# Performance work log

Measured on AMD Instinct MI355X. Metric: run time of the kernel, lower is better.

The kernel has to match this reference:

```python
import jax, jax.numpy as jnp
import numpy as np

B, S, HID = 2, 2048, 2048
H = 16
NOPE, ROPE, VD = 128, 64, 128
QHD = NOPE + ROPE  # 192
KV_RANK = 512
MAX_POS = 2048
EPS = 1e-6


def _rotate_half(x):
    d = x.shape[-1] // 2
    return jnp.concatenate([-x[..., d:], x[..., :d]], axis=-1)


def setup_inputs() -> dict:
    key = jax.random.key(0)
    ks = jax.random.split(key, 8)
    hidden_states = jax.random.normal(ks[0], (B, S, HID), dtype=jnp.float32)
    position_ids = jax.random.randint(ks[1], (B, S), 0, MAX_POS)
    # real RoPE tables
    inv_freq = 1.0 / (10000.0 ** (np.arange(0, ROPE, 2, dtype=np.float32) / ROPE))
    t = np.arange(MAX_POS, dtype=np.float32)
    freqs = np.outer(t, inv_freq)                      # [MAX_POS, ROPE/2]
    emb = np.concatenate([freqs, freqs], axis=-1)      # [MAX_POS, ROPE]
    cos = jnp.asarray(np.cos(emb), dtype=jnp.float32)
    sin = jnp.asarray(np.sin(emb), dtype=jnp.float32)
    sc = lambda fan_in: 1.0 / np.sqrt(fan_in)
    W_q = jax.random.normal(ks[2], (HID, H * QHD), dtype=jnp.float32) * sc(HID)
    W_kva = jax.random.normal(ks[3], (HID, KV_RANK + ROPE), dtype=jnp.float32) * sc(HID)
    ln_g = jnp.ones((KV_RANK,), dtype=jnp.float32)
    ln_b = jnp.zeros((KV_RANK,), dtype=jnp.float32)
    W_kvb = jax.random.normal(ks[4], (KV_RANK, H * (NOPE + VD)), dtype=jnp.float32) * sc(KV_RANK)
    W_o = jax.random.normal(ks[5], (H * VD, HID), dtype=jnp.float32) * sc(H * VD)
    return {"hidden_states": hidden_states, "position_ids": position_ids,
            "cos": cos, "sin": sin, "W_q": W_q, "W_kva": W_kva,
            "ln_g": ln_g, "ln_b": ln_b, "W_kvb": W_kvb, "W_o": W_o}


def _layernorm(x, g, b):
    mu = jnp.mean(x, axis=-1, keepdims=True)
    var = jnp.mean(jnp.square(x - mu), axis=-1, keepdims=True)
    return (x - mu) * jax.lax.rsqrt(var + EPS) * g + b


def reference(hidden_states, position_ids, cos, sin, W_q, W_kva, ln_g, ln_b, W_kvb, W_o):
    bsz, q_len, _ = hidden_states.shape
    # Q projection -> split nope/rope
    q = (hidden_states @ W_q).reshape(bsz, q_len, H, QHD)      # [b,s,h,192]
    q_nope, q_pe = q[..., :NOPE], q[..., NOPE:]
    # compressed KV + shared rope key
    ckv = hidden_states @ W_kva                                 # [b,s,512+64]
    compressed_kv, k_pe = ckv[..., :KV_RANK], ckv[..., KV_RANK:]
    k_pe = k_pe[:, :, None, :]                                  # [b,s,1,64]
    kv = (_layernorm(compressed_kv, ln_g, ln_b) @ W_kvb).reshape(bsz, q_len, H, NOPE + VD)
    k_nope, value_states = kv[..., :NOPE], kv[..., NOPE:]
    # RoPE
    cos_p = cos[position_ids][:, :, None, :]                    # [b,s,1,64]
    sin_p = sin[position_ids][:, :, None, :]
    q_pe = q_pe * cos_p + _rotate_half(q_pe) * sin_p
    k_pe = k_pe * cos_p + _rotate_half(k_pe) * sin_p
    query = jnp.concatenate([q_nope, q_pe], axis=-1)            # [b,s,h,192]
    key = jnp.concatenate([k_nope, jnp.broadcast_to(k_pe, k_nope.shape[:-1] + (ROPE,))], axis=-1)
    # causal attention (FlashMLA math, dense reference)
    scale = 1.0 / jnp.sqrt(jnp.float32(QHD))
    scores = jnp.einsum('bqhd,bkhd->bhqk', query, key) * scale  # [b,h,s,s]
    causal = jnp.tril(jnp.ones((q_len, q_len), dtype=bool))
    scores = jnp.where(causal[None, None], scores, jnp.finfo(scores.dtype).min)
    attn = jax.nn.softmax(scores, axis=-1)
    out = jnp.einsum('bhqk,bkhd->bqhd', attn, value_states)     # [b,s,h,128]
    out = out.reshape(bsz, q_len, H * VD)
    # NOTE: source applies o_proj twice (kept for faithfulness; HID == H*VD)
    out = out @ W_o
    out = out @ W_o
    return out
```

## Files before the change

### kernel.cpp

```cpp
#include <hip/hip_runtime.h>

typedef __bf16 bf16;
typedef __bf16 bf16x4 __attribute__((ext_vector_type(4)));
typedef __bf16 bf16x8 __attribute__((ext_vector_type(8)));
typedef float  f32x4  __attribute__((ext_vector_type(4)));

__device__ __forceinline__ f32x4 mfma16(bf16x8 a, bf16x8 b, f32x4 c) {
  return __builtin_amdgcn_mfma_f32_16x16x32_bf16(a, b, c, 0, 0, 0);
}
__device__ __forceinline__ void load_lds16(const void* g, void* l) {
  __builtin_amdgcn_global_load_lds((__attribute__((address_space(1))) void*)(g),
                                   (__attribute__((address_space(3))) void*)(l),
                                   16, 0, 0);
}

__global__ void cast_bf16(const float* __restrict__ s, bf16* __restrict__ d, int n4) {
  int i = blockIdx.x * blockDim.x + threadIdx.x;
  if (i < n4) {
    float4 v = ((const float4*)s)[i];
    bf16x4 o = { (bf16)v.x, (bf16)v.y, (bf16)v.z, (bf16)v.w };
    *(bf16x4*)(d + (size_t)i * 4) = o;
  }
}

__global__ void transpose_cast(const float* __restrict__ src, bf16* __restrict__ dst,
                               int K, int N, int Npad) {
  __shared__ float tile[32][33];
  const int n0 = blockIdx.x * 32, k0 = blockIdx.y * 32;
  const int tx = threadIdx.x, ty = threadIdx.y;
#pragma unroll
  for (int i = 0; i < 4; ++i) {
    int k = k0 + ty + i * 8, n = n0 + tx;
    tile[ty + i * 8][tx] = (k < K && n < N) ? src[(size_t)k * N + n] : 0.f;
  }
  __syncthreads();
#pragma unroll
  for (int i = 0; i < 4; ++i) {
    int n = n0 + ty + i * 8, k = k0 + tx;
    if (n < Npad && k < K) dst[(size_t)n * K + k] = (bf16)tile[tx][ty + i * 8];
  }
}

template <typename OutT>
__global__ __launch_bounds__(512) void gemm2_bt(
    const bf16* __restrict__ A, const bf16* __restrict__ Bt, OutT* __restrict__ C,
    int M, int N, int K, int GBM, int GBN) {
  __shared__ alignas(16) bf16 As[2][256 * 32];
  __shared__ alignas(16) bf16 Bs[2][128 * 32];
  const int wg = blockIdx.x;
  const int gsz = 8 * GBN;
  const int g = wg / gsz, rem = wg % gsz;
  const int bm = g * 8 + (rem % 8);
  const int bn = rem / 8;

  const int tid = threadIdx.x, wid = tid >> 6, lane = tid & 63;
  const int wr = wid >> 1, wc = wid & 1;
  const int lo = lane & 15, hi = lane >> 4;
  const int w64 = wid * 64;

  f32x4 acc[4][4];
#pragma unroll
  for (int m = 0; m < 4; ++m)
#pragma unroll
    for (int n = 0; n < 4; ++n) acc[m][n] = f32x4{0.f, 0.f, 0.f, 0.f};

  const bf16* Abase = A + (size_t)(bm * 256) * K;
  const bf16* Bbase = Bt + (size_t)(bn * 128) * K;

  auto stage = [&](int buf, int kt) {
    int c = w64 + lane;
    load_lds16(Abase + (size_t)(c >> 2) * K + kt + (c & 3) * 8,
               &As[buf][0] + (size_t)w64 * 8);
    int c2 = 512 + w64 + lane;
    load_lds16(Abase + (size_t)(c2 >> 2) * K + kt + (c2 & 3) * 8,
               &As[buf][0] + (size_t)(512 + w64) * 8);
    load_lds16(Bbase + (size_t)(c >> 2) * K + kt + (c & 3) * 8,
               &Bs[buf][0] + (size_t)w64 * 8);
  };

  const int nt = K >> 5;
  stage(0, 0);
  __syncthreads();
  int cur = 0;
  for (int t = 0; t < nt; ++t) {
    if (t + 1 < nt) stage(cur ^ 1, (t + 1) << 5);
    bf16x8 af[4], bfr[4];
#pragma unroll
    for (int m = 0; m < 4; ++m)
      af[m] = *(const bf16x8*)(&As[cur][0] + (size_t)(wr * 64 + m * 16 + lo) * 32 + hi * 8);
#pragma unroll
    for (int n = 0; n < 4; ++n)
      bfr[n] = *(const bf16x8*)(&Bs[cur][0] + (size_t)(wc * 64 + n * 16 + lo) * 32 + hi * 8);
#pragma unroll
    for (int m = 0; m < 4; ++m)
#pragma unroll
      for (int n = 0; n < 4; ++n) acc[m][n] = mfma16(af[m], bfr[n], acc[m][n]);
    __syncthreads();
    cur ^= 1;
  }
#pragma unroll
  for (int m = 0; m < 4; ++m)
#pragma unroll
    for (int n = 0; n < 4; ++n)
#pragma unroll
      for (int r = 0; r < 4; ++r) {
        int row = bm * 256 + wr * 64 + m * 16 + hi * 4 + r;
        int col = bn * 128 + wc * 64 + n * 16 + lo;
        C[(size_t)row * N + col] = (OutT)acc[m][n][r];
      }
}

template <typename OutT>
__global__ __launch_bounds__(256) void gemm1g_bt(
    const bf16* __restrict__ A, const bf16* __restrict__ Bt, OutT* __restrict__ C,
    int M, int N, int K, int GBN) {
  __shared__ alignas(16) bf16 As[128 * 32];
  __shared__ alignas(16) bf16 Bs[128 * 32];
  const int wg = blockIdx.x;
  const int gsz = 8 * GBN;
  const int g = wg / gsz, rem = wg % gsz;
  const int bm = g * 8 + (rem & 7);
  const int bn = rem >> 3;
  const int tid = threadIdx.x, wid = tid >> 6, lane = tid & 63;
  const int wr = wid >> 1, wc = wid & 1;
  const int lo = lane & 15, hi = lane >> 4;
  f32x4 acc[4][4];
#pragma unroll
  for (int m = 0; m < 4; ++m)
#pragma unroll
    for (int n = 0; n < 4; ++n) acc[m][n] = f32x4{0.f, 0.f, 0.f, 0.f};

  const bf16* Abase = A + (size_t)(bm * 128) * K;
  const bf16* Bbase = Bt + (size_t)(bn * 128) * K;

  for (int kt = 0; kt < K; kt += 32) {
    __syncthreads();
    for (int c0 = wid * 64; c0 < 512; c0 += 256) {
      int c = c0 + lane;
      int row = c >> 2, kc = c & 3;
      load_lds16(Abase + (size_t)row * K + kt + kc * 8, As + (size_t)c0 * 8);
      load_lds16(Bbase + (size_t)row * K + kt + kc * 8, Bs + (size_t)c0 * 8);
    }
    __syncthreads();
    bf16x8 af[4], bfr[4];
#pragma unroll
    for (int m = 0; m < 4; ++m)
      af[m] = *(const bf16x8*)(As + (size_t)(wr * 64 + m * 16 + lo) * 32 + hi * 8);
#pragma unroll
    for (int n = 0; n < 4; ++n)
      bfr[n] = *(const bf16x8*)(Bs + (size_t)(wc * 64 + n * 16 + lo) * 32 + hi * 8);
#pragma unroll
    for (int m = 0; m < 4; ++m)
#pragma unroll
      for (int n = 0; n < 4; ++n) acc[m][n] = mfma16(af[m], bfr[n], acc[m][n]);
  }
#pragma unroll
  for (int m = 0; m < 4; ++m)
#pragma unroll
    for (int n = 0; n < 4; ++n)
#pragma unroll
      for (int r = 0; r < 4; ++r) {
        int row = bm * 128 + wr * 64 + m * 16 + hi * 4 + r;
        int col = bn * 128 + wc * 64 + n * 16 + lo;
        C[(size_t)row * N + col] = (OutT)acc[m][n][r];
      }
}

__global__ __launch_bounds__(256) void ln_rope(
    const bf16* __restrict__ QKVb, const float* __restrict__ g, const float* __restrict__ bta,
    const int* __restrict__ pos, const float* __restrict__ cosT, const float* __restrict__ sinT,
    bf16* __restrict__ LNout, float* __restrict__ KPE) {
  const int row = blockIdx.x, tid = threadIdx.x;
  const bf16* x = QKVb + (size_t)row * 3712 + 3072;
  float v0 = (float)x[tid], v1 = (float)x[tid + 256];
  float s = v0 + v1, s2 = v0 * v0 + v1 * v1;
#pragma unroll
  for (int off = 1; off < 64; off <<= 1) {
    s += __shfl_xor(s, off, 64);
    s2 += __shfl_xor(s2, off, 64);
  }
  __shared__ float red[8];
  const int wid = tid >> 6;
  if ((tid & 63) == 0) { red[wid] = s; red[4 + wid] = s2; }
  __syncthreads();
  s = red[0] + red[1] + red[2] + red[3];
  s2 = red[4] + red[5] + red[6] + red[7];
  const float mu = s * (1.f / 512.f);
  const float var = s2 * (1.f / 512.f) - mu * mu;
  const float rstd = rsqrtf(var + 1e-6f);
  LNout[(size_t)row * 512 + tid] = (bf16)((v0 - mu) * rstd * g[tid] + bta[tid]);
  LNout[(size_t)row * 512 + tid + 256] = (bf16)((v1 - mu) * rstd * g[tid + 256] + bta[tid + 256]);
  if (tid < 64) {
    float kvp = (float)x[512 + tid];
    float partner = (float)x[512 + (tid ^ 32)];
    float rot = (tid < 32) ? -partner : partner;
    int p = pos[row];
    KPE[(size_t)row * 64 + tid] = kvp * cosT[p * 64 + tid] + rot * sinT[p * 64 + tid];
  }
}

__global__ void pack_k(const bf16* __restrict__ KVb, const float* __restrict__ KPE,
                       bf16* __restrict__ Kh) {
  const int h = blockIdx.x, row = blockIdx.y;
  const int t = threadIdx.x;
  const bf16* kv = KVb + (size_t)row * 4096 + h * 256;
  bf16* o = Kh + ((size_t)((row >> 11) * 16 + h) * 2048 + (row & 2047)) * 200;
  o[t] = kv[t];
  o[t + 64] = kv[t + 64];
  o[128 + t] = (bf16)KPE[(size_t)row * 64 + t];
  if (t < 8) o[192 + t] = (bf16)0.f;
}

__global__ void transpose_v(const bf16* __restrict__ KVb, bf16* __restrict__ Vt) {
  __shared__ bf16 tile[32][33];
  const int bh = blockIdx.x, st = blockIdx.y, dt = blockIdx.z;
  const int b = bh >> 4, h = bh & 15;
  const int tx = threadIdx.x, ty = threadIdx.y;
#pragma unroll
  for (int i = 0; i < 4; ++i) {
    int sIdx = st * 32 + ty + i * 8;
    tile[ty + i * 8][tx] = KVb[(size_t)(b * 2048 + sIdx) * 4096 + h * 256 + 128 + dt * 32 + tx];
  }
  __syncthreads();
  const int kt = st >> 1;
  const int kvl = (st & 1) * 32;
#pragma unroll
  for (int i = 0; i < 4; ++i) {
    int d = dt * 32 + ty + i * 8;
    size_t rowbase = ((size_t)(bh * 32 + kt) * 128 + d) * 72;
    Vt[rowbase + kvl + tx] = tile[tx][ty + i * 8];
    if ((st & 1) && tx < 8) Vt[rowbase + 64 + tx] = (bf16)0.f;
  }
}

__global__ __launch_bounds__(256, 3) void flash_attn(
    const bf16* __restrict__ QKVb, const int* __restrict__ pos,
    const float* __restrict__ cosT, const float* __restrict__ sinT,
    const bf16* __restrict__ Kh, const bf16* __restrict__ Vt,
    bf16* __restrict__ Ob) {
  __shared__ alignas(16) bf16 Ks[64 * 200];
  __shared__ alignas(16) bf16 Vs[128 * 72];
  __shared__ alignas(16) bf16 Ps[4][16 * 72];
  const int bh = blockIdx.x, qt = 31 - blockIdx.y;
  const int b = bh >> 4, h = bh & 15;
  const int tid = threadIdx.x, wid = tid >> 6, lane = tid & 63;
  const int lo = lane & 15, hi = lane >> 4;
  const int q0 = qt * 64 + wid * 16;

  bf16x8 qf[6];
  {
    const int grow_i = b * 2048 + q0 + lo;
    const bf16* qsrc = QKVb + (size_t)grow_i * 3712 + h * 192 + hi * 8;
    bf16x8 raw[6];
#pragma unroll
    for (int kg = 0; kg < 6; ++kg) raw[kg] = *(const bf16x8*)(qsrc + kg * 32);
    const float scale = 0.07216878364870322f;
#pragma unroll
    for (int kg = 0; kg < 4; ++kg)
#pragma unroll
      for (int j = 0; j < 8; ++j) qf[kg][j] = (bf16)((float)raw[kg][j] * scale);
    const int p = pos[grow_i];
    const float* cb = cosT + p * 64 + hi * 8;
    const float* sb = sinT + p * 64 + hi * 8;
#pragma unroll
    for (int j = 0; j < 8; ++j) {
      float q4 = (float)raw[4][j], q5 = (float)raw[5][j];
      qf[4][j] = (bf16)((q4 * cb[j] - q5 * sb[j]) * scale);
      qf[5][j] = (bf16)((q5 * cb[32 + j] + q4 * sb[32 + j]) * scale);
    }
  }
  float m_r[4] = {-INFINITY, -INFINITY, -INFINITY, -INFINITY};
  f32x4 accl = f32x4{0.f, 0.f, 0.f, 0.f};
  f32x4 acc[8];
#pragma unroll
  for (int v = 0; v < 8; ++v) acc[v] = f32x4{0.f, 0.f, 0.f, 0.f};
  const bf16 one_b = (bf16)1.f;
  const bf16x8 ones = {one_b, one_b, one_b, one_b, one_b, one_b, one_b, one_b};

  const bf16* Kbase = Kh + (size_t)bh * 2048 * 200;
  const bf16* Vbase = Vt + (size_t)bh * 32 * (128 * 72);
  bf16* Pw = &Ps[wid][0];

  const int last = qt * 64;
  for (int kv0 = 0; kv0 <= last; kv0 += 64) {
    {
      const bf16* srcK = Kbase + (size_t)kv0 * 200;
      for (int c0 = wid * 64; c0 < 1600; c0 += 256)
        load_lds16(srcK + (size_t)(c0 + lane) * 8, Ks + (size_t)c0 * 8);
      const bf16* srcV = Vbase + (size_t)(kv0 >> 6) * (128 * 72);
      for (int c0 = wid * 64; c0 < 1152; c0 += 256)
        load_lds16(srcV + (size_t)(c0 + lane) * 8, Vs + (size_t)c0 * 8);
    }
    __syncthreads();

    f32x4 sacc[4];
    __builtin_amdgcn_s_setprio(1);
#pragma unroll
    for (int nk = 0; nk < 4; ++nk) {
      sacc[nk] = f32x4{0.f, 0.f, 0.f, 0.f};
#pragma unroll
      for (int kg = 0; kg < 6; ++kg) {
        bf16x8 kf = *(const bf16x8*)(Ks + (size_t)(nk * 16 + lo) * 200 + kg * 32 + hi * 8);
        sacc[nk] = mfma16(qf[kg], kf, sacc[nk]);
      }
    }
    __builtin_amdgcn_s_setprio(0);
    if (kv0 == last) {
#pragma unroll
      for (int nk = 0; nk < 4; ++nk)
#pragma unroll
        for (int r = 0; r < 4; ++r)
          if (kv0 + nk * 16 + lo > q0 + hi * 4 + r) sacc[nk][r] = -INFINITY;
    }
    float mx[4];
#pragma unroll
    for (int r = 0; r < 4; ++r) {
      float m0 = fmaxf(fmaxf(sacc[0][r], sacc[1][r]), fmaxf(sacc[2][r], sacc[3][r]));
      m0 = fmaxf(m0, __shfl_xor(m0, 1, 64));
      m0 = fmaxf(m0, __shfl_xor(m0, 2, 64));
      m0 = fmaxf(m0, __shfl_xor(m0, 4, 64));
      m0 = fmaxf(m0, __shfl_xor(m0, 8, 64));
      mx[r] = m0;
    }
    bool grow = !(mx[0] <= m_r[0] + 8.f && mx[1] <= m_r[1] + 8.f &&
                  mx[2] <= m_r[2] + 8.f && mx[3] <= m_r[3] + 8.f);
    if (__any(grow)) {
#pragma unroll
      for (int r = 0; r < 4; ++r) {
        float mnew = fmaxf(m_r[r], mx[r]);
        float sc = __expf(m_r[r] - mnew);
        m_r[r] = mnew;
        accl[r] *= sc;
#pragma unroll
        for (int v = 0; v < 8; ++v) acc[v][r] *= sc;
      }
    }
#pragma unroll
    for (int nk = 0; nk < 4; ++nk)
#pragma unroll
      for (int r = 0; r < 4; ++r) {
        float p = __expf(sacc[nk][r] - m_r[r]);
        Pw[(hi * 4 + r) * 72 + nk * 16 + lo] = (bf16)p;
      }
    bf16x8 pf0 = *(const bf16x8*)(Pw + (size_t)lo * 72 + hi * 8);
    bf16x8 pf1 = *(const bf16x8*)(Pw + (size_t)lo * 72 + 32 + hi * 8);
    __builtin_amdgcn_s_setprio(1);
    accl = mfma16(pf0, ones, accl);
    accl = mfma16(pf1, ones, accl);
#pragma unroll
    for (int v = 0; v < 8; ++v) {
      const bf16* vrow = Vs + (size_t)(v * 16 + lo) * 72 + hi * 8;
      bf16x8 vf0 = *(const bf16x8*)(vrow);
      bf16x8 vf1 = *(const bf16x8*)(vrow + 32);
      acc[v] = mfma16(pf0, vf0, acc[v]);
      acc[v] = mfma16(pf1, vf1, acc[v]);
    }
    __builtin_amdgcn_s_setprio(0);
    __syncthreads();
  }
#pragma unroll
  for (int r = 0; r < 4; ++r) {
    float invl = 1.f / accl[r];
    int qrow = q0 + hi * 4 + r;
    bf16* orow = Ob + ((size_t)b * 2048 + qrow) * 2048 + h * 128 + lo;
#pragma unroll
    for (int v = 0; v < 8; ++v) orow[v * 16] = (bf16)(acc[v][r] * invl);
  }
}

extern "C" void kernel_launch(void* const* d_in, const int* in_sizes, int n_in,
                              void* d_out, int out_size, void* d_ws, size_t ws_size,
                              hipStream_t stream) {
  const float* hidden = (const float*)d_in[0];
  const int* pos = (const int*)d_in[1];
  const float* cosT = (const float*)d_in[2];
  const float* sinT = (const float*)d_in[3];
  const float* W_q = (const float*)d_in[4];
  const float* W_kva = (const float*)d_in[5];
  const float* g = (const float*)d_in[6];
  const float* bta = (const float*)d_in[7];
  const float* W_kvb = (const float*)d_in[8];
  const float* W_o = (const float*)d_in[9];
  float* out = (float*)d_out;

  char* w = (char*)d_ws;
  size_t used = 0;
  auto carve = [&](size_t bytes) -> char* {
    char* p = w;
    size_t pad = (bytes + 255) & ~(size_t)255;
    w += pad;
    used += pad;
    return p;
  };
  bf16* Xb = (bf16*)carve(16777216);
  bf16* Wqkva_t = (bf16*)carve(15204352);
  bf16* Wkvb_t = (bf16*)carve(4194304);
  bf16* Wo_t = (bf16*)carve(8388608);
  bf16* QKVb = (bf16*)carve(30408704);
  bf16* Ob = (bf16*)carve(16777216);
  bf16* LNout = (bf16*)carve(4194304);
  float* KPE = (float*)carve(1048576);
  char* KVT1 = carve(33554432);
  bf16* KVb = (bf16*)KVT1;
  bf16* T1b = (bf16*)KVT1;
  bf16* Kh = (bf16*)carve(26214400);
  bf16* Vt = (bf16*)carve(18874368);

  if (used > ws_size) return;

  cast_bf16<<<8192, 256, 0, stream>>>(hidden, Xb, 2097152);
  transpose_cast<<<dim3(96, 64), dim3(32, 8), 0, stream>>>(W_q, Wqkva_t, 2048, 3072, 3072);
  transpose_cast<<<dim3(20, 64), dim3(32, 8), 0, stream>>>(W_kva, Wqkva_t + (size_t)3072 * 2048,
                                                           2048, 576, 640);
  transpose_cast<<<dim3(128, 16), dim3(32, 8), 0, stream>>>(W_kvb, Wkvb_t, 512, 4096, 4096);
  transpose_cast<<<dim3(64, 64), dim3(32, 8), 0, stream>>>(W_o, Wo_t, 2048, 2048, 2048);

  gemm2_bt<bf16><<<16 * 29, 512, 0, stream>>>(Xb, Wqkva_t, QKVb, 4096, 3712, 2048, 16, 29);
  ln_rope<<<4096, 256, 0, stream>>>(QKVb, g, bta, pos, cosT, sinT, LNout, KPE);
  gemm2_bt<bf16><<<16 * 32, 512, 0, stream>>>(LNout, Wkvb_t, KVb, 4096, 4096, 512, 16, 32);
  pack_k<<<dim3(16, 4096), 64, 0, stream>>>(KVb, KPE, Kh);
  transpose_v<<<dim3(32, 64, 4), dim3(32, 8), 0, stream>>>(KVb, Vt);
  flash_attn<<<dim3(32, 32), 256, 0, stream>>>(QKVb, pos, cosT, sinT, Kh, Vt, Ob);
  gemm1g_bt<bf16><<<32 * 16, 256, 0, stream>>>(Ob, Wo_t, T1b, 4096, 2048, 2048, 16);
  gemm1g_bt<float><<<32 * 16, 256, 0, stream>>>(T1b, Wo_t, out, 4096, 2048, 2048, 16);
}
```

Measured before the change: 353.9 us.

## Pair complementary causal query tiles per attention block to balance work and share KV loads

Each flash-attention block now handles two query tiles, pi and 31-pi, so every block does about the same amount of causal work, and the grid is halved. The K/V tiles loaded into LDS are shared by both query tiles while the lower tile is still active, so the short tile adds no extra global loads. The cost is double the accumulator and Q-fragment registers, so the launch-bounds occupancy hint of 3 is dropped. That raises register pressure and likely lowers occupancy, and 512 blocks may underfill the GPU.

```diff
diff --git a/kernel.cpp b/kernel.cpp
--- a/kernel.cpp
+++ b/kernel.cpp
@@ -233,7 +233,7 @@
   }
 }
 
-__global__ __launch_bounds__(256, 3) void flash_attn(
+__global__ __launch_bounds__(256) void flash_attn(
     const bf16* __restrict__ QKVb, const int* __restrict__ pos,
     const float* __restrict__ cosT, const float* __restrict__ sinT,
     const bf16* __restrict__ Kh, const bf16* __restrict__ Vt,
@@ -241,20 +241,22 @@
   __shared__ alignas(16) bf16 Ks[64 * 200];
   __shared__ alignas(16) bf16 Vs[128 * 72];
   __shared__ alignas(16) bf16 Ps[4][16 * 72];
-  const int bh = blockIdx.x, qt = 31 - blockIdx.y;
+  const int bh = blockIdx.x, pi = blockIdx.y;
+  const int qtA = pi, qtB = 31 - pi;
   const int b = bh >> 4, h = bh & 15;
   const int tid = threadIdx.x, wid = tid >> 6, lane = tid & 63;
   const int lo = lane & 15, hi = lane >> 4;
-  const int q0 = qt * 64 + wid * 16;
-
-  bf16x8 qf[6];
-  {
-    const int grow_i = b * 2048 + q0 + lo;
+  const int q0A = qtA * 64 + wid * 16;
+  const int q0B = qtB * 64 + wid * 16;
+
+  const float scale = 0.07216878364870322f;
+  bf16x8 qfA[6], qfB[6];
+  auto loadQ = [&](int q0w, bf16x8* qf) {
+    const int grow_i = b * 2048 + q0w + lo;
     const bf16* qsrc = QKVb + (size_t)grow_i * 3712 + h * 192 + hi * 8;
     bf16x8 raw[6];
 #pragma unroll
     for (int kg = 0; kg < 6; ++kg) raw[kg] = *(const bf16x8*)(qsrc + kg * 32);
-    const float scale = 0.07216878364870322f;
 #pragma unroll
     for (int kg = 0; kg < 4; ++kg)
 #pragma unroll
@@ -268,12 +270,20 @@
       qf[4][j] = (bf16)((q4 * cb[j] - q5 * sb[j]) * scale);
       qf[5][j] = (bf16)((q5 * cb[32 + j] + q4 * sb[32 + j]) * scale);
     }
-  }
-  float m_r[4] = {-INFINITY, -INFINITY, -INFINITY, -INFINITY};
-  f32x4 accl = f32x4{0.f, 0.f, 0.f, 0.f};
-  f32x4 acc[8];
-#pragma unroll
-  for (int v = 0; v < 8; ++v) acc[v] = f32x4{0.f, 0.f, 0.f, 0.f};
+  };
+  loadQ(q0A, qfA);
+  loadQ(q0B, qfB);
+
+  float m_rA[4], m_rB[4];
+#pragma unroll
+  for (int r = 0; r < 4; ++r) { m_rA[r] = -INFINITY; m_rB[r] = -INFINITY; }
+  f32x4 acclA = f32x4{0.f, 0.f, 0.f, 0.f}, acclB = f32x4{0.f, 0.f, 0.f, 0.f};
+  f32x4 accA[8], accB[8];
+#pragma unroll
+  for (int v = 0; v < 8; ++v) {
+    accA[v] = f32x4{0.f, 0.f, 0.f, 0.f};
+    accB[v] = f32x4{0.f, 0.f, 0.f, 0.f};
+  }
   const bf16 one_b = (bf16)1.f;
   const bf16x8 ones = {one_b, one_b, one_b, one_b, one_b, one_b, one_b, one_b};
 
@@ -281,8 +291,63 @@
   const bf16* Vbase = Vt + (size_t)bh * 32 * (128 * 72);
   bf16* Pw = &Ps[wid][0];
 
-  const int last = qt * 64;
-  for (int kv0 = 0; kv0 <= last; kv0 += 64) {
+  auto softmax_pv = [&](f32x4* sacc, float* m_r, f32x4& accl, f32x4* acc,
+                        int q0w, bool diag, int kv0) {
+    if (diag) {
+#pragma unroll
+      for (int nk = 0; nk < 4; ++nk)
+#pragma unroll
+        for (int r = 0; r < 4; ++r)
+          if (kv0 + nk * 16 + lo > q0w + hi * 4 + r) sacc[nk][r] = -INFINITY;
+    }
+    float mx[4];
+#pragma unroll
+    for (int r = 0; r < 4; ++r) {
+      float m0 = fmaxf(fmaxf(sacc[0][r], sacc[1][r]), fmaxf(sacc[2][r], sacc[3][r]));
+      m0 = fmaxf(m0, __shfl_xor(m0, 1, 64));
+      m0 = fmaxf(m0, __shfl_xor(m0, 2, 64));
+      m0 = fmaxf(m0, __shfl_xor(m0, 4, 64));
+      m0 = fmaxf(m0, __shfl_xor(m0, 8, 64));
+      mx[r] = m0;
+    }
+    bool grow_ = !(mx[0] <= m_r[0] + 8.f && mx[1] <= m_r[1] + 8.f &&
+                   mx[2] <= m_r[2] + 8.f && mx[3] <= m_r[3] + 8.f);
+    if (__any(grow_)) {
+#pragma unroll
+      for (int r = 0; r < 4; ++r) {
+        float mnew = fmaxf(m_r[r], mx[r]);
+        float sc = __expf(m_r[r] - mnew);
+        m_r[r] = mnew;
+        accl[r] *= sc;
+#pragma unroll
+        for (int v = 0; v < 8; ++v) acc[v][r] *= sc;
+      }
+    }
+#pragma unroll
+    for (int nk = 0; nk < 4; ++nk)
+#pragma unroll
+      for (int r = 0; r < 4; ++r) {
+        float p = __expf(sacc[nk][r] - m_r[r]);
+        Pw[(hi * 4 + r) * 72 + nk * 16 + lo] = (bf16)p;
+      }
+    bf16x8 pf0 = *(const bf16x8*)(Pw + (size_t)lo * 72 + hi * 8);
+    bf16x8 pf1 = *(const bf16x8*)(Pw + (size_t)lo * 72 + 32 + hi * 8);
+    __builtin_amdgcn_s_setprio(1);
+    accl = mfma16(pf0, ones, accl);
+    accl = mfma16(pf1, ones, accl);
+#pragma unroll
+    for (int v = 0; v < 8; ++v) {
+      const bf16* vrow = Vs + (size_t)(v * 16 + lo) * 72 + hi * 8;
+      bf16x8 vf0 = *(const bf16x8*)(vrow);
+      bf16x8 vf1 = *(const bf16x8*)(vrow + 32);
+      acc[v] = mfma16(pf0, vf0, acc[v]);
+      acc[v] = mfma16(pf1, vf1, acc[v]);
+    }
+    __builtin_amdgcn_s_setprio(0);
+  };
+
+  const int lastA = qtA * 64, lastB = qtB * 64;
+  for (int kv0 = 0; kv0 <= lastB; kv0 += 64) {
     {
       const bf16* srcK = Kbase + (size_t)kv0 * 200;
       for (int c0 = wid * 64; c0 < 1600; c0 += 256)
@@ -293,79 +358,51 @@
     }
     __syncthreads();
 
-    f32x4 sacc[4];
+    const bool actA = (kv0 <= lastA);
+    f32x4 saccA[4], saccB[4];
     __builtin_amdgcn_s_setprio(1);
-#pragma unroll
-    for (int nk = 0; nk < 4; ++nk) {
-      sacc[nk] = f32x4{0.f, 0.f, 0.f, 0.f};
-#pragma unroll
-      for (int kg = 0; kg < 6; ++kg) {
-        bf16x8 kf = *(const bf16x8*)(Ks + (size_t)(nk * 16 + lo) * 200 + kg * 32 + hi * 8);
-        sacc[nk] = mfma16(qf[kg], kf, sacc[nk]);
+    if (actA) {
+#pragma unroll
+      for (int nk = 0; nk < 4; ++nk) {
+        saccA[nk] = f32x4{0.f, 0.f, 0.f, 0.f};
+        saccB[nk] = f32x4{0.f, 0.f, 0.f, 0.f};
+#pragma unroll
+        for (int kg = 0; kg < 6; ++kg) {
+          bf16x8 kf = *(const bf16x8*)(Ks + (size_t)(nk * 16 + lo) * 200 + kg * 32 + hi * 8);
+          saccA[nk] = mfma16(qfA[kg], kf, saccA[nk]);
+          saccB[nk] = mfma16(qfB[kg], kf, saccB[nk]);
+        }
+      }
+    } else {
+#pragma unroll
+      for (int nk = 0; nk < 4; ++nk) {
+        saccB[nk] = f32x4{0.f, 0.f, 0.f, 0.f};
+#pragma unroll
+        for (int kg = 0; kg < 6; ++kg) {
+          bf16x8 kf = *(const bf16x8*)(Ks + (size_t)(nk * 16 + lo) * 200 + kg * 32 + hi * 8);
+          saccB[nk] = mfma16(qfB[kg], kf, saccB[nk]);
+        }
       }
     }
     __builtin_amdgcn_s_setprio(0);
-    if (kv0 == last) {
-#pragma unroll
-      for (int nk = 0; nk < 4; ++nk)
-#pragma unroll
-        for (int r = 0; r < 4; ++r)
-          if (kv0 + nk * 16 + lo > q0 + hi * 4 + r) sacc[nk][r] = -INFINITY;
-    }
-    float mx[4];
+
+    if (actA) softmax_pv(saccA, m_rA, acclA, accA, q0A, kv0 == lastA, kv0);
+    softmax_pv(saccB, m_rB, acclB, accB, q0B, kv0 == lastB, kv0);
+
+    __syncthreads();
+  }
+  auto epilogue = [&](f32x4& accl, f32x4* acc, int q0w) {
 #pragma unroll
     for (int r = 0; r < 4; ++r) {
-      float m0 = fmaxf(fmaxf(sacc[0][r], sacc[1][r]), fmaxf(sacc[2][r], sacc[3][r]));
-      m0 = fmaxf(m0, __shfl_xor(m0, 1, 64));
-      m0 = fmaxf(m0, __shfl_xor(m0, 2, 64));
-      m0 = fmaxf(m0, __shfl_xor(m0, 4, 64));
-      m0 = fmaxf(m0, __shfl_xor(m0, 8, 64));
-      mx[r] = m0;
-    }
-    bool grow = !(mx[0] <= m_r[0] + 8.f && mx[1] <= m_r[1] + 8.f &&
-                  mx[2] <= m_r[2] + 8.f && mx[3] <= m_r[3] + 8.f);
-    if (__any(grow)) {
-#pragma unroll
-      for (int r = 0; r < 4; ++r) {
-        float mnew = fmaxf(m_r[r], mx[r]);
-        float sc = __expf(m_r[r] - mnew);
-        m_r[r] = mnew;
-        accl[r] *= sc;
-#pragma unroll
-        for (int v = 0; v < 8; ++v) acc[v][r] *= sc;
-      }
-    }
-#pragma unroll
-    for (int nk = 0; nk < 4; ++nk)
-#pragma unroll
-      for (int r = 0; r < 4; ++r) {
-        float p = __expf(sacc[nk][r] - m_r[r]);
-        Pw[(hi * 4 + r) * 72 + nk * 16 + lo] = (bf16)p;
-      }
-    bf16x8 pf0 = *(const bf16x8*)(Pw + (size_t)lo * 72 + hi * 8);
-    bf16x8 pf1 = *(const bf16x8*)(Pw + (size_t)lo * 72 + 32 + hi * 8);
-    __builtin_amdgcn_s_setprio(1);
-    accl = mfma16(pf0, ones, accl);
-    accl = mfma16(pf1, ones, accl);
-#pragma unroll
-    for (int v = 0; v < 8; ++v) {
-      const bf16* vrow = Vs + (size_t)(v * 16 + lo) * 72 + hi * 8;
-      bf16x8 vf0 = *(const bf16x8*)(vrow);
-      bf16x8 vf1 = *(const bf16x8*)(vrow + 32);
-      acc[v] = mfma16(pf0, vf0, acc[v]);
-      acc[v] = mfma16(pf1, vf1, acc[v]);
-    }
-    __builtin_amdgcn_s_setprio(0);
-    __syncthreads();
-  }
-#pragma unroll
-  for (int r = 0; r < 4; ++r) {
-    float invl = 1.f / accl[r];
-    int qrow = q0 + hi * 4 + r;
-    bf16* orow = Ob + ((size_t)b * 2048 + qrow) * 2048 + h * 128 + lo;
-#pragma unroll
-    for (int v = 0; v < 8; ++v) orow[v * 16] = (bf16)(acc[v][r] * invl);
-  }
+      float invl = 1.f / accl[r];
+      int qrow = q0w + hi * 4 + r;
+      bf16* orow = Ob + ((size_t)b * 2048 + qrow) * 2048 + h * 128 + lo;
+#pragma unroll
+      for (int v = 0; v < 8; ++v) orow[v * 16] = (bf16)(acc[v][r] * invl);
+    }
+  };
+  epilogue(acclA, accA, q0A);
+  epilogue(acclB, accB, q0B);
 }
 
 extern "C" void kernel_launch(void* const* d_in, const int* in_sizes, int n_in,
@@ -420,7 +457,7 @@
   gemm2_bt<bf16><<<16 * 32, 512, 0, stream>>>(LNout, Wkvb_t, KVb, 4096, 4096, 512, 16, 32);
   pack_k<<<dim3(16, 4096), 64, 0, stream>>>(KVb, KPE, Kh);
   transpose_v<<<dim3(32, 64, 4), dim3(32, 8), 0, stream>>>(KVb, Vt);
-  flash_attn<<<dim3(32, 32), 256, 0, stream>>>(QKVb, pos, cosT, sinT, Kh, Vt, Ob);
+  flash_attn<<<dim3(32, 16), 256, 0, stream>>>(QKVb, pos, cosT, sinT, Kh, Vt, Ob);
   gemm1g_bt<bf16><<<32 * 16, 256, 0, stream>>>(Ob, Wo_t, T1b, 4096, 2048, 2048, 16);
   gemm1g_bt<float><<<32 * 16, 256, 0, stream>>>(T1b, Wo_t, out, 4096, 2048, 2048, 16);
 }
```

New measurement: 402.3 us. +13.7%, slower.
